# Kernel tuning notes

Measured on AMD Instinct MI355X. Metric: run time of the kernel, lower is better.

The kernel has to match this reference:

```python
import jax, jax.numpy as jnp
import numpy as np

N_NODES = 100000
N_EDGES = 1600000
N_GRAPHS = 256
D_IN = 128
D_HID = 128
D_OUT = 64


def graph_conv(x, src, dst, W_rel, b_rel, W_root):
    # PyG GraphConv: out = lin_rel(mean_{j->i} x_j) + lin_root(x)
    msgs = jax.ops.segment_sum(x[src], dst, num_segments=N_NODES)  # [N, d]
    deg = jax.ops.segment_sum(jnp.ones((src.shape[0],), x.dtype), dst, num_segments=N_NODES)
    agg = msgs / jnp.maximum(deg, 1.0)[:, None]
    return agg @ W_rel + b_rel + x @ W_root


def setup_inputs() -> dict:
    key = jax.random.key(0)
    ks = jax.random.split(key, 12)
    x = jax.random.normal(ks[0], (N_NODES, D_IN), dtype=jnp.float32)
    edge_index = jax.random.randint(ks[1], (2, N_EDGES), 0, N_NODES, dtype=jnp.int64)
    batch = jnp.sort(jax.random.randint(ks[2], (N_NODES,), 0, N_GRAPHS, dtype=jnp.int64))
    def lin(k, fan_in, fan_out):
        bound = 1.0 / np.sqrt(fan_in)
        return jax.random.uniform(k, (fan_in, fan_out), jnp.float32, -bound, bound)
    inp = {
        "x": x, "edge_index": edge_index, "batch": batch,
        "W1_rel": lin(ks[3], D_IN, D_HID), "b1_rel": jnp.zeros((D_HID,), jnp.float32), "W1_root": lin(ks[4], D_IN, D_HID),
        "W2_rel": lin(ks[5], D_HID, D_HID), "b2_rel": jnp.zeros((D_HID,), jnp.float32), "W2_root": lin(ks[6], D_HID, D_HID),
        "W3_rel": lin(ks[7], D_HID, D_HID), "b3_rel": jnp.zeros((D_HID,), jnp.float32), "W3_root": lin(ks[8], D_HID, D_HID),
        "Wl": lin(ks[9], D_HID, D_OUT), "bl": jnp.zeros((D_OUT,), jnp.float32),
    }
    return inp


def reference(x, edge_index, batch, W1_rel, b1_rel, W1_root, W2_rel, b2_rel, W2_root,
              W3_rel, b3_rel, W3_root, Wl, bl):
    src, dst = edge_index[0], edge_index[1]
    h = jax.nn.relu(graph_conv(x, src, dst, W1_rel, b1_rel, W1_root))
    h = jax.nn.relu(graph_conv(h, src, dst, W2_rel, b2_rel, W2_root))
    h = graph_conv(h, src, dst, W3_rel, b3_rel, W3_root)
    # global mean pool over graphs
    sums = jax.ops.segment_sum(h, batch, num_segments=N_GRAPHS)          # [G, d]
    cnts = jax.ops.segment_sum(jnp.ones((h.shape[0],), h.dtype), batch, num_segments=N_GRAPHS)
    pooled = sums / jnp.maximum(cnts, 1.0)[:, None]
    # dropout is identity at inference
    return pooled @ Wl + bl  # [G, D_OUT]
```

## Files before the change

kernel.cpp:

```cpp
#include <hip/hip_runtime.h>
#include <hip/hip_bf16.h>

#define N_NODES  100000
#define N_EDGES  1600000
#define N_GRAPHS 256
#define DCH      128
#define DOUT     64
#define NB       391
#define PADB     512
#define SLACK    4608
#define CHUNK    2048

typedef short v8s __attribute__((ext_vector_type(8)));
typedef float v4f __attribute__((ext_vector_type(4)));

static __device__ __forceinline__ float bf2f(unsigned short u) {
    unsigned int x = ((unsigned int)u) << 16;
    return __builtin_bit_cast(float, x);
}
static __device__ __forceinline__ unsigned short f2bf(float f) {
    unsigned int x = __builtin_bit_cast(unsigned int, f);
    unsigned int r = (x + 0x7fffu + ((x >> 16) & 1u)) >> 16;
    return (unsigned short)r;
}
static __device__ __forceinline__ int clampi(int v, int lo, int hi) {
    return v < lo ? lo : (v > hi ? hi : v);
}

__global__ void __launch_bounds__(256) binA_kernel(const int* __restrict__ src, const int* __restrict__ dst,
                                                   int* __restrict__ gcur, uint2* __restrict__ region) {
    __shared__ uint2 stage[CHUNK];
    __shared__ int hcnt[PADB], hcnt2[PADB], hoff[PADB], garr[PADB];
    __shared__ int s2[256];
    int tid = threadIdx.x;
    int e0  = blockIdx.x * CHUNK;
    int nedge = N_EDGES - e0; if (nedge > CHUNK) nedge = CHUNK;

    for (int b = tid; b < PADB; b += 256) { hcnt[b] = 0; hcnt2[b] = 0; }
    __syncthreads();

    int es[CHUNK / 256], ed[CHUNK / 256];
    #pragma unroll
    for (int j = 0; j < CHUNK / 256; j++) {
        int e = e0 + j * 256 + tid;
        if (e < N_EDGES) {
            es[j] = clampi(src[e], 0, N_NODES - 1);
            ed[j] = clampi(dst[e], 0, N_NODES - 1);
            atomicAdd(&hcnt[ed[j] >> 8], 1);
        } else { es[j] = -1; ed[j] = 0; }
    }
    __syncthreads();

    int v0 = hcnt[2 * tid], v1 = hcnt[2 * tid + 1];
    s2[tid] = v0 + v1; __syncthreads();
    for (int off = 1; off < 256; off <<= 1) {
        int x = (tid >= off) ? s2[tid - off] : 0;
        __syncthreads();
        s2[tid] += x;
        __syncthreads();
    }
    int excl = s2[tid] - (v0 + v1);
    hoff[2 * tid] = excl; hoff[2 * tid + 1] = excl + v0;
    __syncthreads();

    for (int b = tid; b < NB; b += 256) {
        int c = hcnt[b];
        garr[b] = b * SLACK + ((c > 0) ? atomicAdd(&gcur[b], c) : 0);
    }
    __syncthreads();

    #pragma unroll
    for (int j = 0; j < CHUNK / 256; j++) {
        if (es[j] >= 0) {
            int b = ed[j] >> 8;
            int pos = atomicAdd(&hcnt2[b], 1) + hoff[b];
            stage[pos] = (uint2){(unsigned)es[j], (unsigned)ed[j]};
        }
    }
    __syncthreads();

    for (int i = tid; i < nedge; i += 256) {
        uint2 en = stage[i];
        int b = (int)(en.y >> 8);
        int gpos = garr[b] + (i - hoff[b]);
        if (gpos < (b + 1) * SLACK) region[gpos] = en;
    }
}

__global__ void __launch_bounds__(256) scan_kernel(const int* __restrict__ gcur,
                                                   int* __restrict__ hoffG, int* __restrict__ rowptr) {
    __shared__ int s2[256];
    int tid = threadIdx.x;
    int c0 = gcur[2 * tid];     if (c0 > SLACK) c0 = SLACK;
    int c1 = gcur[2 * tid + 1]; if (c1 > SLACK) c1 = SLACK;
    s2[tid] = c0 + c1; __syncthreads();
    for (int off = 1; off < 256; off <<= 1) {
        int x = (tid >= off) ? s2[tid - off] : 0;
        __syncthreads();
        s2[tid] += x;
        __syncthreads();
    }
    int excl = s2[tid] - (c0 + c1);
    hoffG[2 * tid] = excl; hoffG[2 * tid + 1] = excl + c0;
    if (tid == 255) rowptr[N_NODES] = s2[255];
}

__global__ void __launch_bounds__(256) binFinish_kernel(const uint2* __restrict__ region, const int* __restrict__ gcur,
                                                        const int* __restrict__ hoffG,
                                                        int* __restrict__ rowptr, int* __restrict__ csr) {
    __shared__ int h[256], sc[256], cur[256];
    int b = blockIdx.x, tid = threadIdx.x;
    h[tid] = 0;
    int base = hoffG[b];
    int size = gcur[b]; if (size > SLACK) size = SLACK;
    int node0 = b * 256;
    __syncthreads();
    for (int j = tid; j < size; j += 256) {
        unsigned loc = region[b * SLACK + j].y - (unsigned)node0;
        if (loc < 256u) atomicAdd(&h[loc], 1);
    }
    __syncthreads();
    int v = h[tid]; sc[tid] = v; __syncthreads();
    for (int off = 1; off < 256; off <<= 1) {
        int x = (tid >= off) ? sc[tid - off] : 0;
        __syncthreads();
        sc[tid] += x;
        __syncthreads();
    }
    int myptr = base + sc[tid] - v;
    int node = node0 + tid;
    if (node < N_NODES) rowptr[node] = myptr;
    cur[tid] = myptr;
    __syncthreads();
    for (int j = tid; j < size; j += 256) {
        uint2 en = region[b * SLACK + j];
        unsigned loc = en.y - (unsigned)node0;
        if (loc < 256u) {
            int p = atomicAdd(&cur[loc], 1);
            if (p >= 0 && p < N_EDGES) csr[p] = (int)en.x;
        }
    }
}

__global__ void __launch_bounds__(256) prep_kernel(const float* __restrict__ x, unsigned short* __restrict__ B2,
                                                   const float* __restrict__ W1rel, const float* __restrict__ W1root,
                                                   const float* __restrict__ W2rel, const float* __restrict__ W2root,
                                                   const float* __restrict__ W3rel, const float* __restrict__ W3root,
                                                   unsigned short* __restrict__ frag,
                                                   unsigned short* __restrict__ z1, unsigned short* __restrict__ z2) {
    int bid = blockIdx.x, tid = threadIdx.x;
    if (bid < 12500) {
        size_t i = ((size_t)bid * 256 + tid) * 4;
        float4 f = *reinterpret_cast<const float4*>(x + i);
        uint2 o;
        o.x = ((unsigned)f2bf(f.y) << 16) | (unsigned)f2bf(f.x);
        o.y = ((unsigned)f2bf(f.w) << 16) | (unsigned)f2bf(f.z);
        *reinterpret_cast<uint2*>(B2 + i) = o;
    } else if (bid < 12548) {
        int gid = (bid - 12500) * 256 + tid;
        int lane = gid & 63;
        int nt   = (gid >> 6) & 7;
        int kt   = (gid >> 9) & 7;
        int L    = gid >> 12;
        const float* rel  = (L == 0) ? W1rel  : (L == 1) ? W2rel  : W3rel;
        const float* root = (L == 0) ? W1root : (L == 1) ? W2root : W3root;
        int n  = nt * 16 + (lane & 15);
        int k0 = kt * 32 + (lane >> 4) * 8;
        unsigned short o[8];
        #pragma unroll
        for (int j = 0; j < 8; j++) {
            int k = k0 + j;
            float w = (k < 128) ? rel[k * 128 + n] : root[(k - 128) * 128 + n];
            o[j] = f2bf(w);
        }
        uint4 u;
        u.x = (unsigned)o[0] | ((unsigned)o[1] << 16);
        u.y = (unsigned)o[2] | ((unsigned)o[3] << 16);
        u.z = (unsigned)o[4] | ((unsigned)o[5] << 16);
        u.w = (unsigned)o[6] | ((unsigned)o[7] << 16);
        *reinterpret_cast<uint4*>(frag + (size_t)gid * 8) = u;
    } else {
        if (tid < 64)       reinterpret_cast<unsigned*>(z1)[tid] = 0;
        else if (tid < 128) reinterpret_cast<unsigned*>(z2)[tid - 64] = 0;
    }
}

__global__ void __launch_bounds__(256, 6) layer_kernel(
    const unsigned short* __restrict__ hin,
    const int* __restrict__ rowptr, const int* __restrict__ csr,
    const unsigned short* __restrict__ frag, const float* __restrict__ bias,
    unsigned short* __restrict__ hout,
    const int* __restrict__ batch, float* __restrict__ psum, int mode)
{
    __shared__ __attribute__((aligned(16))) unsigned short As[4][16 * DCH];
    const int wave = threadIdx.x >> 6;
    const int lane = threadIdx.x & 63;
    const int l16  = lane & 15;
    const int quad = lane >> 4;
    const int base = blockIdx.x * 64 + wave * 16;
    if (base >= N_NODES) return;

    char* Asb = reinterpret_cast<char*>(As[wave]);

    int ridx = base + (lane < 17 ? lane : 16);
    if (ridx > N_NODES) ridx = N_NODES;
    int rp = rowptr[ridx];
    const int R0 = __builtin_amdgcn_readlane(rp, 0);
    const int R1 = __builtin_amdgcn_readlane(rp, 16);

    int ni     = 0;
    int nstart = R0;
    int nend   = __builtin_amdgcn_readlane(rp, 1);
    float a0 = 0.f, a1 = 0.f;

    int t0  = csr[R0 + l16];
    int idx = (R0 + l16 < R1) ? t0 : N_NODES;

    for (int e0 = R0; e0 < R1; e0 += 16) {
        int en   = e0 + 16 + l16;
        int tn   = csr[en];
        int idxn = (en < R1) ? tn : N_NODES;

        unsigned v[16];
        #pragma unroll
        for (int j = 0; j < 16; j++) {
            int s = __builtin_amdgcn_readlane(idx, j);
            v[j] = *reinterpret_cast<const unsigned*>(hin + (size_t)s * DCH + lane * 2);
        }

        #pragma unroll
        for (int j = 0; j < 16; j++) {
            int e = e0 + j;
            while (ni < 16 && e == nend) {
                int deg = nend - nstart;
                float inv = 1.0f / (float)(deg > 1 ? deg : 1);
                unsigned o = ((unsigned)f2bf(a1 * inv) << 16) | (unsigned)f2bf(a0 * inv);
                *reinterpret_cast<unsigned*>(Asb + ni * 256 + ((lane * 4) ^ ((ni & 7) << 4))) = o;
                a0 = 0.f; a1 = 0.f;
                ni++;
                nstart = nend;
                nend = __builtin_amdgcn_readlane(rp, ni + 1 < 17 ? ni + 1 : 16);
            }
            a0 += bf2f((unsigned short)(v[j] & 0xffffu));
            a1 += bf2f((unsigned short)(v[j] >> 16));
        }
        idx = idxn;
    }
    while (ni < 16) {
        int deg = nend - nstart;
        float inv = 1.0f / (float)(deg > 1 ? deg : 1);
        unsigned o = ((unsigned)f2bf(a1 * inv) << 16) | (unsigned)f2bf(a0 * inv);
        *reinterpret_cast<unsigned*>(Asb + ni * 256 + ((lane * 4) ^ ((ni & 7) << 4))) = o;
        a0 = 0.f; a1 = 0.f;
        ni++;
        nstart = nend;
        nend = __builtin_amdgcn_readlane(rp, ni + 1 < 17 ? ni + 1 : 16);
    }

    v4f acc[8];
    #pragma unroll
    for (int nt = 0; nt < 8; nt++) acc[nt] = (v4f){0.f, 0.f, 0.f, 0.f};

    #pragma unroll
    for (int kt = 0; kt < 8; kt++) {
        v8s av;
        if (kt < 4) {
            int co = (kt * 64 + quad * 16) ^ ((l16 & 7) << 4);
            av = *reinterpret_cast<const v8s*>(Asb + l16 * 256 + co);
        } else {
            int ak = (kt - 4) * 32 + quad * 8;
            int row = base + l16; if (row > N_NODES) row = N_NODES;
            av = *reinterpret_cast<const v8s*>(hin + (size_t)row * DCH + ak);
        }
        #pragma unroll
        for (int nt = 0; nt < 8; nt++) {
            v8s b = *reinterpret_cast<const v8s*>(frag + (((size_t)(kt * 8 + nt)) * 64 + lane) * 8);
            acc[nt] = __builtin_amdgcn_mfma_f32_16x16x32_bf16(av, b, acc[nt], 0, 0, 0);
        }
    }

    if (mode != 2) {
        #pragma unroll
        for (int nt = 0; nt < 8; nt++) {
            int n = nt * 16 + l16;
            float bv = bias[n];
            #pragma unroll
            for (int r = 0; r < 4; r++) {
                int row = base + quad * 4 + r;
                if (row < N_NODES) {
                    float v = acc[nt][r] + bv;
                    if (mode == 1) v = fmaxf(v, 0.f);
                    hout[(size_t)row * DCH + n] = f2bf(v);
                }
            }
        }
    } else {
        int last = base + 15;
        bool fast = (last < N_NODES) && (batch[base] == batch[last]);
        if (fast) {
            int g = batch[base];
            #pragma unroll
            for (int nt = 0; nt < 8; nt++) {
                int n = nt * 16 + l16;
                float s = acc[nt][0] + acc[nt][1] + acc[nt][2] + acc[nt][3] + 4.0f * bias[n];
                s += __shfl_xor(s, 16);
                s += __shfl_xor(s, 32);
                if (quad == 0) atomicAdd(&psum[g * DCH + n], s);
            }
        } else {
            int g[4];
            #pragma unroll
            for (int r = 0; r < 4; r++) {
                int row = base + quad * 4 + r;
                g[r] = (row < N_NODES) ? batch[row] : -1;
            }
            #pragma unroll
            for (int nt = 0; nt < 8; nt++) {
                int n = nt * 16 + l16;
                float bv = bias[n];
                float s = 0.f; int cg = -1;
                #pragma unroll
                for (int r = 0; r < 4; r++) {
                    if (g[r] < 0) continue;
                    if (g[r] != cg) {
                        if (cg >= 0) atomicAdd(&psum[cg * DCH + n], s);
                        s = 0.f; cg = g[r];
                    }
                    s += acc[nt][r] + bv;
                }
                if (cg >= 0) atomicAdd(&psum[cg * DCH + n], s);
            }
        }
    }
}

static __device__ __forceinline__ int lowerb(const int* __restrict__ a, int n, int key) {
    int lo = 0, hi = n;
    while (lo < hi) { int mid = (lo + hi) >> 1; if (a[mid] < key) lo = mid + 1; else hi = mid; }
    return lo;
}

__global__ void __launch_bounds__(64) final_kernel(const float* __restrict__ psum,
                                                   const int* __restrict__ batch,
                                                   const float* __restrict__ Wl, const float* __restrict__ bl,
                                                   float* __restrict__ out) {
    __shared__ float ps[DCH];
    __shared__ int bounds[2];
    int g = blockIdx.x, tid = threadIdx.x;
    if (tid == 0) {
        bounds[0] = lowerb(batch, N_NODES, g);
        bounds[1] = lowerb(batch, N_NODES, g + 1);
    }
    __syncthreads();
    int cnt = bounds[1] - bounds[0];
    float inv = 1.0f / (float)(cnt > 1 ? cnt : 1);
    ps[tid] = psum[g * DCH + tid] * inv;
    ps[tid + 64] = psum[g * DCH + tid + 64] * inv;
    __syncthreads();
    float o = 0.f;
    #pragma unroll 4
    for (int c = 0; c < DCH; c++) o += ps[c] * Wl[c * DOUT + tid];
    out[g * DOUT + tid] = o + bl[tid];
}

extern "C" void kernel_launch(void* const* d_in, const int* in_sizes, int n_in,
                              void* d_out, int out_size, void* d_ws, size_t ws_size,
                              hipStream_t stream) {
    const float* x     = (const float*)d_in[0];
    const int*   edge  = (const int*)d_in[1];
    const int*   src   = edge;
    const int*   dst   = edge + N_EDGES;
    const int*   batch = (const int*)d_in[2];
    const float* W1rel  = (const float*)d_in[3];
    const float* b1     = (const float*)d_in[4];
    const float* W1root = (const float*)d_in[5];
    const float* W2rel  = (const float*)d_in[6];
    const float* b2     = (const float*)d_in[7];
    const float* W2root = (const float*)d_in[8];
    const float* W3rel  = (const float*)d_in[9];
    const float* b3     = (const float*)d_in[10];
    const float* W3root = (const float*)d_in[11];
    const float* Wl     = (const float*)d_in[12];
    const float* bl     = (const float*)d_in[13];
    float* out = (float*)d_out;

    char* ws = (char*)d_ws;
    size_t off = 0;
    auto carve = [&](size_t bytes) -> void* {
        void* p = ws + off;
        off += (bytes + 255) & ~(size_t)255;
        return p;
    };
    int*            rowptr  = (int*)carve((size_t)(N_NODES + 1) * 4);
    int*            csr     = (int*)carve((size_t)(N_EDGES + 64) * 4);
    int*            gcur    = (int*)carve((size_t)PADB * 4 + (size_t)N_GRAPHS * DCH * 4);
    float*          psum    = (float*)(gcur + PADB);
    int*            hoffG   = (int*)carve((size_t)PADB * 4);
    unsigned short* frag    = (unsigned short*)carve((size_t)3 * 8 * 8 * 64 * 8 * 2);
    unsigned short* B1      = (unsigned short*)carve((size_t)(N_NODES + 1) * DCH * 2);
    unsigned short* B2      = (unsigned short*)carve((size_t)(N_NODES + 1) * DCH * 2);
    uint2*          region  = (uint2*)B1;

    hipMemsetAsync(gcur, 0, (size_t)PADB * 4 + (size_t)N_GRAPHS * DCH * 4, stream);

    binA_kernel<<<(N_EDGES + CHUNK - 1) / CHUNK, 256, 0, stream>>>(src, dst, gcur, region);
    scan_kernel<<<1, 256, 0, stream>>>(gcur, hoffG, rowptr);
    binFinish_kernel<<<NB, 256, 0, stream>>>(region, gcur, hoffG, rowptr, csr);
    prep_kernel<<<12549, 256, 0, stream>>>(x, B2, W1rel, W1root, W2rel, W2root, W3rel, W3root,
                                           frag, B1 + (size_t)N_NODES * DCH, B2 + (size_t)N_NODES * DCH);

    const int layerGrid = (N_NODES + 63) / 64;

    layer_kernel<<<layerGrid, 256, 0, stream>>>(B2, rowptr, csr, frag,         b1, B1, batch, psum, 1);
    layer_kernel<<<layerGrid, 256, 0, stream>>>(B1, rowptr, csr, frag + 32768, b2, B2, batch, psum, 1);
    layer_kernel<<<layerGrid, 256, 0, stream>>>(B2, rowptr, csr, frag + 65536, b3, B1, batch, psum, 2);

    final_kernel<<<N_GRAPHS, 64, 0, stream>>>(psum, batch, Wl, bl, out);
}
```

Measured before the change: 411.4 us.

## Double-buffer neighbor gathers in layer kernel and fold memset into prep

The aggregation loop in the layer kernel now ping-pongs between two register buffers. It issues the next 16-edge chunk's row gathers and the following chunk's CSR index load before reducing the current chunk, so global-load latency overlaps the accumulation. The CSR padding is enlarged to cover the deeper index lookahead. The separate hipMemsetAsync is removed: the prep kernel now zeroes gcur and psum itself and is launched before the binning kernels, saving an API call. The extra 16-register buffer raises VGPR pressure under the 6-blocks-per-SM launch bound, which could cost occupancy or cause spills.

```diff
diff --git a/kernel.cpp b/kernel.cpp
--- a/kernel.cpp
+++ b/kernel.cpp
@@ -147,7 +147,8 @@
                                                    const float* __restrict__ W2rel, const float* __restrict__ W2root,
                                                    const float* __restrict__ W3rel, const float* __restrict__ W3root,
                                                    unsigned short* __restrict__ frag,
-                                                   unsigned short* __restrict__ z1, unsigned short* __restrict__ z2) {
+                                                   unsigned short* __restrict__ z1, unsigned short* __restrict__ z2,
+                                                   int* __restrict__ gcur, float* __restrict__ psum) {
     int bid = blockIdx.x, tid = threadIdx.x;
     if (bid < 12500) {
         size_t i = ((size_t)bid * 256 + tid) * 4;
@@ -179,9 +180,13 @@
         u.z = (unsigned)o[4] | ((unsigned)o[5] << 16);
         u.w = (unsigned)o[6] | ((unsigned)o[7] << 16);
         *reinterpret_cast<uint4*>(frag + (size_t)gid * 8) = u;
-    } else {
+    } else if (bid == 12548) {
         if (tid < 64)       reinterpret_cast<unsigned*>(z1)[tid] = 0;
         else if (tid < 128) reinterpret_cast<unsigned*>(z2)[tid - 64] = 0;
+        gcur[tid] = 0; gcur[tid + 256] = 0;
+    } else {
+        int i = (bid - 12549) * 1024 + tid * 4;
+        *reinterpret_cast<float4*>(psum + i) = (float4){0.f, 0.f, 0.f, 0.f};
     }
 }
 
@@ -213,38 +218,80 @@
     int nend   = __builtin_amdgcn_readlane(rp, 1);
     float a0 = 0.f, a1 = 0.f;
 
-    int t0  = csr[R0 + l16];
-    int idx = (R0 + l16 < R1) ? t0 : N_NODES;
-
-    for (int e0 = R0; e0 < R1; e0 += 16) {
-        int en   = e0 + 16 + l16;
-        int tn   = csr[en];
-        int idxn = (en < R1) ? tn : N_NODES;
-
-        unsigned v[16];
+    int nch = (R1 - R0 + 15) >> 4;
+    if (nch < 1) nch = 1;
+    const int nch2 = (nch + 1) & ~1;
+
+    unsigned vA[16], vB[16];
+
+    int tA = csr[R0 + l16];
+    int tB;
+    {
+        int idx = (R0 + l16 < R1) ? tA : N_NODES;
         #pragma unroll
         for (int j = 0; j < 16; j++) {
             int s = __builtin_amdgcn_readlane(idx, j);
-            v[j] = *reinterpret_cast<const unsigned*>(hin + (size_t)s * DCH + lane * 2);
-        }
-
-        #pragma unroll
-        for (int j = 0; j < 16; j++) {
-            int e = e0 + j;
-            while (ni < 16 && e == nend) {
-                int deg = nend - nstart;
-                float inv = 1.0f / (float)(deg > 1 ? deg : 1);
-                unsigned o = ((unsigned)f2bf(a1 * inv) << 16) | (unsigned)f2bf(a0 * inv);
-                *reinterpret_cast<unsigned*>(Asb + ni * 256 + ((lane * 4) ^ ((ni & 7) << 4))) = o;
-                a0 = 0.f; a1 = 0.f;
-                ni++;
-                nstart = nend;
-                nend = __builtin_amdgcn_readlane(rp, ni + 1 < 17 ? ni + 1 : 16);
-            }
-            a0 += bf2f((unsigned short)(v[j] & 0xffffu));
-            a1 += bf2f((unsigned short)(v[j] >> 16));
-        }
-        idx = idxn;
+            vA[j] = *reinterpret_cast<const unsigned*>(hin + (size_t)s * DCH + lane * 2);
+        }
+        tB = csr[R0 + 16 + l16];
+    }
+
+    int e0 = R0;
+    for (int c = 0; c < nch2; c += 2) {
+        {
+            int e1 = e0 + 16;
+            int idx = (e1 + l16 < R1) ? tB : N_NODES;
+            #pragma unroll
+            for (int j = 0; j < 16; j++) {
+                int s = __builtin_amdgcn_readlane(idx, j);
+                vB[j] = *reinterpret_cast<const unsigned*>(hin + (size_t)s * DCH + lane * 2);
+            }
+            tA = csr[e0 + 32 + l16];
+            #pragma unroll
+            for (int j = 0; j < 16; j++) {
+                int e = e0 + j;
+                while (ni < 16 && e == nend) {
+                    int deg = nend - nstart;
+                    float inv = 1.0f / (float)(deg > 1 ? deg : 1);
+                    unsigned o = ((unsigned)f2bf(a1 * inv) << 16) | (unsigned)f2bf(a0 * inv);
+                    *reinterpret_cast<unsigned*>(Asb + ni * 256 + ((lane * 4) ^ ((ni & 7) << 4))) = o;
+                    a0 = 0.f; a1 = 0.f;
+                    ni++;
+                    nstart = nend;
+                    nend = __builtin_amdgcn_readlane(rp, ni + 1 < 17 ? ni + 1 : 16);
+                }
+                a0 += bf2f((unsigned short)(vA[j] & 0xffffu));
+                a1 += bf2f((unsigned short)(vA[j] >> 16));
+            }
+            e0 = e1;
+        }
+        {
+            int e1 = e0 + 16;
+            int idx = (e1 + l16 < R1) ? tA : N_NODES;
+            #pragma unroll
+            for (int j = 0; j < 16; j++) {
+                int s = __builtin_amdgcn_readlane(idx, j);
+                vA[j] = *reinterpret_cast<const unsigned*>(hin + (size_t)s * DCH + lane * 2);
+            }
+            tB = csr[e0 + 32 + l16];
+            #pragma unroll
+            for (int j = 0; j < 16; j++) {
+                int e = e0 + j;
+                while (ni < 16 && e == nend) {
+                    int deg = nend - nstart;
+                    float inv = 1.0f / (float)(deg > 1 ? deg : 1);
+                    unsigned o = ((unsigned)f2bf(a1 * inv) << 16) | (unsigned)f2bf(a0 * inv);
+                    *reinterpret_cast<unsigned*>(Asb + ni * 256 + ((lane * 4) ^ ((ni & 7) << 4))) = o;
+                    a0 = 0.f; a1 = 0.f;
+                    ni++;
+                    nstart = nend;
+                    nend = __builtin_amdgcn_readlane(rp, ni + 1 < 17 ? ni + 1 : 16);
+                }
+                a0 += bf2f((unsigned short)(vB[j] & 0xffffu));
+                a1 += bf2f((unsigned short)(vB[j] >> 16));
+            }
+            e0 = e1;
+        }
     }
     while (ni < 16) {
         int deg = nend - nstart;
@@ -392,7 +439,7 @@
         return p;
     };
     int*            rowptr  = (int*)carve((size_t)(N_NODES + 1) * 4);
-    int*            csr     = (int*)carve((size_t)(N_EDGES + 64) * 4);
+    int*            csr     = (int*)carve((size_t)(N_EDGES + 128) * 4);
     int*            gcur    = (int*)carve((size_t)PADB * 4 + (size_t)N_GRAPHS * DCH * 4);
     float*          psum    = (float*)(gcur + PADB);
     int*            hoffG   = (int*)carve((size_t)PADB * 4);
@@ -401,13 +448,13 @@
     unsigned short* B2      = (unsigned short*)carve((size_t)(N_NODES + 1) * DCH * 2);
     uint2*          region  = (uint2*)B1;
 
-    hipMemsetAsync(gcur, 0, (size_t)PADB * 4 + (size_t)N_GRAPHS * DCH * 4, stream);
+    prep_kernel<<<12581, 256, 0, stream>>>(x, B2, W1rel, W1root, W2rel, W2root, W3rel, W3root,
+                                           frag, B1 + (size_t)N_NODES * DCH, B2 + (size_t)N_NODES * DCH,
+                                           gcur, psum);
 
     binA_kernel<<<(N_EDGES + CHUNK - 1) / CHUNK, 256, 0, stream>>>(src, dst, gcur, region);
     scan_kernel<<<1, 256, 0, stream>>>(gcur, hoffG, rowptr);
     binFinish_kernel<<<NB, 256, 0, stream>>>(region, gcur, hoffG, rowptr, csr);
-    prep_kernel<<<12549, 256, 0, stream>>>(x, B2, W1rel, W1root, W2rel, W2root, W3rel, W3root,
-                                           frag, B1 + (size_t)N_NODES * DCH, B2 + (size_t)N_NODES * DCH);
 
     const int layerGrid = (N_NODES + 63) / 64;
 
```

Result: no change. 411.0 us (-0.1%).

## Triple-buffer neighbor gathers in layer kernel and fold memset into prep kernel

Applied to the files above, without the earlier changes.

The CSR aggregation loop in layer_kernel now keeps three 16-edge gather buffers in flight. While one chunk is accumulated, loads for the next chunks are already issued, which hides gather latency. Launch bounds drop from 6 to 4 waves per SIMD to fit the extra registers, and the CSR allocation is padded for the lookahead reads. Separately, the hipMemsetAsync of gcur and psum is replaced by extra blocks in prep_kernel, which now launches first, removing one API call and launch.

```diff
diff --git a/kernel.cpp b/kernel.cpp
--- a/kernel.cpp
+++ b/kernel.cpp
@@ -147,7 +147,8 @@
                                                    const float* __restrict__ W2rel, const float* __restrict__ W2root,
                                                    const float* __restrict__ W3rel, const float* __restrict__ W3root,
                                                    unsigned short* __restrict__ frag,
-                                                   unsigned short* __restrict__ z1, unsigned short* __restrict__ z2) {
+                                                   unsigned short* __restrict__ z1, unsigned short* __restrict__ z2,
+                                                   int* __restrict__ gcur, float* __restrict__ psum) {
     int bid = blockIdx.x, tid = threadIdx.x;
     if (bid < 12500) {
         size_t i = ((size_t)bid * 256 + tid) * 4;
@@ -179,13 +180,17 @@
         u.z = (unsigned)o[4] | ((unsigned)o[5] << 16);
         u.w = (unsigned)o[6] | ((unsigned)o[7] << 16);
         *reinterpret_cast<uint4*>(frag + (size_t)gid * 8) = u;
-    } else {
+    } else if (bid == 12548) {
         if (tid < 64)       reinterpret_cast<unsigned*>(z1)[tid] = 0;
         else if (tid < 128) reinterpret_cast<unsigned*>(z2)[tid - 64] = 0;
-    }
-}
-
-__global__ void __launch_bounds__(256, 6) layer_kernel(
+        gcur[tid] = 0; gcur[tid + 256] = 0;
+    } else {
+        int i = (bid - 12549) * 1024 + tid * 4;
+        *reinterpret_cast<float4*>(psum + i) = (float4){0.f, 0.f, 0.f, 0.f};
+    }
+}
+
+__global__ void __launch_bounds__(256, 4) layer_kernel(
     const unsigned short* __restrict__ hin,
     const int* __restrict__ rowptr, const int* __restrict__ csr,
     const unsigned short* __restrict__ frag, const float* __restrict__ bias,
@@ -213,24 +218,25 @@
     int nend   = __builtin_amdgcn_readlane(rp, 1);
     float a0 = 0.f, a1 = 0.f;
 
-    int t0  = csr[R0 + l16];
-    int idx = (R0 + l16 < R1) ? t0 : N_NODES;
-
-    for (int e0 = R0; e0 < R1; e0 += 16) {
-        int en   = e0 + 16 + l16;
-        int tn   = csr[en];
-        int idxn = (en < R1) ? tn : N_NODES;
-
-        unsigned v[16];
+    int nch = (R1 - R0 + 15) >> 4;
+    if (nch < 1) nch = 1;
+    const int nch3 = ((nch + 2) / 3) * 3;
+
+    unsigned v0[16], v1[16], v2[16];
+    int t0, t1, t2;
+
+    auto issue_gathers = [&](unsigned (&vv)[16], int traw, int eb) {
+        int idx = (eb + l16 < R1) ? traw : N_NODES;
         #pragma unroll
         for (int j = 0; j < 16; j++) {
             int s = __builtin_amdgcn_readlane(idx, j);
-            v[j] = *reinterpret_cast<const unsigned*>(hin + (size_t)s * DCH + lane * 2);
-        }
-
+            vv[j] = *reinterpret_cast<const unsigned*>(hin + (size_t)s * DCH + lane * 2);
+        }
+    };
+    auto accum = [&](unsigned (&vv)[16], int eb) {
         #pragma unroll
         for (int j = 0; j < 16; j++) {
-            int e = e0 + j;
+            int e = eb + j;
             while (ni < 16 && e == nend) {
                 int deg = nend - nstart;
                 float inv = 1.0f / (float)(deg > 1 ? deg : 1);
@@ -241,10 +247,32 @@
                 nstart = nend;
                 nend = __builtin_amdgcn_readlane(rp, ni + 1 < 17 ? ni + 1 : 16);
             }
-            a0 += bf2f((unsigned short)(v[j] & 0xffffu));
-            a1 += bf2f((unsigned short)(v[j] >> 16));
-        }
-        idx = idxn;
+            a0 += bf2f((unsigned short)(vv[j] & 0xffffu));
+            a1 += bf2f((unsigned short)(vv[j] >> 16));
+        }
+    };
+
+    t0 = csr[R0 + l16];
+    t1 = csr[R0 + 16 + l16];
+    t2 = csr[R0 + 32 + l16];
+    issue_gathers(v0, t0, R0);
+    t0 = csr[R0 + 48 + l16];
+    issue_gathers(v1, t1, R0 + 16);
+
+    int e0 = R0;
+    for (int c = 0; c < nch3; c += 3) {
+        t1 = csr[e0 + 64 + l16];
+        issue_gathers(v2, t2, e0 + 32);
+        accum(v0, e0);
+        e0 += 16;
+        t2 = csr[e0 + 64 + l16];
+        issue_gathers(v0, t0, e0 + 32);
+        accum(v1, e0);
+        e0 += 16;
+        t0 = csr[e0 + 64 + l16];
+        issue_gathers(v1, t1, e0 + 32);
+        accum(v2, e0);
+        e0 += 16;
     }
     while (ni < 16) {
         int deg = nend - nstart;
@@ -392,7 +420,7 @@
         return p;
     };
     int*            rowptr  = (int*)carve((size_t)(N_NODES + 1) * 4);
-    int*            csr     = (int*)carve((size_t)(N_EDGES + 64) * 4);
+    int*            csr     = (int*)carve((size_t)(N_EDGES + 160) * 4);
     int*            gcur    = (int*)carve((size_t)PADB * 4 + (size_t)N_GRAPHS * DCH * 4);
     float*          psum    = (float*)(gcur + PADB);
     int*            hoffG   = (int*)carve((size_t)PADB * 4);
@@ -401,13 +429,13 @@
     unsigned short* B2      = (unsigned short*)carve((size_t)(N_NODES + 1) * DCH * 2);
     uint2*          region  = (uint2*)B1;
 
-    hipMemsetAsync(gcur, 0, (size_t)PADB * 4 + (size_t)N_GRAPHS * DCH * 4, stream);
+    prep_kernel<<<12581, 256, 0, stream>>>(x, B2, W1rel, W1root, W2rel, W2root, W3rel, W3root,
+                                           frag, B1 + (size_t)N_NODES * DCH, B2 + (size_t)N_NODES * DCH,
+                                           gcur, psum);
 
     binA_kernel<<<(N_EDGES + CHUNK - 1) / CHUNK, 256, 0, stream>>>(src, dst, gcur, region);
     scan_kernel<<<1, 256, 0, stream>>>(gcur, hoffG, rowptr);
     binFinish_kernel<<<NB, 256, 0, stream>>>(region, gcur, hoffG, rowptr, csr);
-    prep_kernel<<<12549, 256, 0, stream>>>(x, B2, W1rel, W1root, W2rel, W2root, W3rel, W3root,
-                                           frag, B1 + (size_t)N_NODES * DCH, B2 + (size_t)N_NODES * DCH);
 
     const int layerGrid = (N_NODES + 63) / 64;
 
```

Result: no change. 414.4 us (+0.7%).

## Split fused layer into per-node aggregation and GEMM kernels, merge setup kernels

Applied to the files above, without the earlier changes.

The fused gather-plus-GEMM layer kernel is split in two. A new aggregation kernel assigns one wave per node and writes the mean-aggregated bf16 features to a buffer. A GEMM kernel then loads that tile into LDS and writes its output in place. Separately, the binning and prep kernels are merged into one launch, and the global scan is recomputed redundantly inside each binFinish block, which removes the standalone scan launch. This aims for better load balance across irregular node degrees and fewer setup launches. The cost is writing and re-reading an extra 128-wide bf16 buffer per layer, three more layer launches, and dropped row bounds checks in the GEMM path.

```diff
diff --git a/kernel.cpp b/kernel.cpp
--- a/kernel.cpp
+++ b/kernel.cpp
@@ -10,6 +10,7 @@
 #define PADB     512
 #define SLACK    4608
 #define CHUNK    2048
+#define NBINA    782
 
 typedef short v8s __attribute__((ext_vector_type(8)));
 typedef float v4f __attribute__((ext_vector_type(4)));
@@ -27,12 +28,60 @@
     return v < lo ? lo : (v > hi ? hi : v);
 }
 
-__global__ void __launch_bounds__(256) binA_kernel(const int* __restrict__ src, const int* __restrict__ dst,
-                                                   int* __restrict__ gcur, uint2* __restrict__ region) {
+__global__ void __launch_bounds__(256) binAprep_kernel(
+    const int* __restrict__ src, const int* __restrict__ dst,
+    int* __restrict__ gcur, uint2* __restrict__ region,
+    const float* __restrict__ x, unsigned short* __restrict__ B2,
+    const float* __restrict__ W1rel, const float* __restrict__ W1root,
+    const float* __restrict__ W2rel, const float* __restrict__ W2root,
+    const float* __restrict__ W3rel, const float* __restrict__ W3root,
+    unsigned short* __restrict__ frag,
+    unsigned short* __restrict__ z1, unsigned short* __restrict__ z2)
+{
     __shared__ uint2 stage[CHUNK];
     __shared__ int hcnt[PADB], hcnt2[PADB], hoff[PADB], garr[PADB];
     __shared__ int s2[256];
     int tid = threadIdx.x;
+
+    if (blockIdx.x >= NBINA) {
+        int bid = blockIdx.x - NBINA;
+        if (bid < 12500) {
+            size_t i = ((size_t)bid * 256 + tid) * 4;
+            float4 f = *reinterpret_cast<const float4*>(x + i);
+            uint2 o;
+            o.x = ((unsigned)f2bf(f.y) << 16) | (unsigned)f2bf(f.x);
+            o.y = ((unsigned)f2bf(f.w) << 16) | (unsigned)f2bf(f.z);
+            *reinterpret_cast<uint2*>(B2 + i) = o;
+        } else if (bid < 12548) {
+            int gid = (bid - 12500) * 256 + tid;
+            int lane = gid & 63;
+            int nt   = (gid >> 6) & 7;
+            int kt   = (gid >> 9) & 7;
+            int L    = gid >> 12;
+            const float* rel  = (L == 0) ? W1rel  : (L == 1) ? W2rel  : W3rel;
+            const float* root = (L == 0) ? W1root : (L == 1) ? W2root : W3root;
+            int n  = nt * 16 + (lane & 15);
+            int k0 = kt * 32 + (lane >> 4) * 8;
+            unsigned short o[8];
+            #pragma unroll
+            for (int j = 0; j < 8; j++) {
+                int k = k0 + j;
+                float w = (k < 128) ? rel[k * 128 + n] : root[(k - 128) * 128 + n];
+                o[j] = f2bf(w);
+            }
+            uint4 u;
+            u.x = (unsigned)o[0] | ((unsigned)o[1] << 16);
+            u.y = (unsigned)o[2] | ((unsigned)o[3] << 16);
+            u.z = (unsigned)o[4] | ((unsigned)o[5] << 16);
+            u.w = (unsigned)o[6] | ((unsigned)o[7] << 16);
+            *reinterpret_cast<uint4*>(frag + (size_t)gid * 8) = u;
+        } else {
+            if (tid < 64)       reinterpret_cast<unsigned*>(z1)[tid] = 0;
+            else if (tid < 128) reinterpret_cast<unsigned*>(z2)[tid - 64] = 0;
+        }
+        return;
+    }
+
     int e0  = blockIdx.x * CHUNK;
     int nedge = N_EDGES - e0; if (nedge > CHUNK) nedge = CHUNK;
 
@@ -54,9 +103,9 @@
     int v0 = hcnt[2 * tid], v1 = hcnt[2 * tid + 1];
     s2[tid] = v0 + v1; __syncthreads();
     for (int off = 1; off < 256; off <<= 1) {
-        int x = (tid >= off) ? s2[tid - off] : 0;
-        __syncthreads();
-        s2[tid] += x;
+        int xx = (tid >= off) ? s2[tid - off] : 0;
+        __syncthreads();
+        s2[tid] += xx;
         __syncthreads();
     }
     int excl = s2[tid] - (v0 + v1);
@@ -87,34 +136,28 @@
     }
 }
 
-__global__ void __launch_bounds__(256) scan_kernel(const int* __restrict__ gcur,
-                                                   int* __restrict__ hoffG, int* __restrict__ rowptr) {
-    __shared__ int s2[256];
-    int tid = threadIdx.x;
+__global__ void __launch_bounds__(256) binFinish_kernel(const uint2* __restrict__ region, const int* __restrict__ gcur,
+                                                        int* __restrict__ rowptr, int* __restrict__ csr) {
+    __shared__ int h[256], sc[256], cur[256], s2[256], hoff[PADB];
+    int b = blockIdx.x, tid = threadIdx.x;
     int c0 = gcur[2 * tid];     if (c0 > SLACK) c0 = SLACK;
     int c1 = gcur[2 * tid + 1]; if (c1 > SLACK) c1 = SLACK;
-    s2[tid] = c0 + c1; __syncthreads();
+    s2[tid] = c0 + c1;
+    h[tid] = 0;
+    __syncthreads();
     for (int off = 1; off < 256; off <<= 1) {
-        int x = (tid >= off) ? s2[tid - off] : 0;
-        __syncthreads();
-        s2[tid] += x;
+        int xx = (tid >= off) ? s2[tid - off] : 0;
+        __syncthreads();
+        s2[tid] += xx;
         __syncthreads();
     }
     int excl = s2[tid] - (c0 + c1);
-    hoffG[2 * tid] = excl; hoffG[2 * tid + 1] = excl + c0;
-    if (tid == 255) rowptr[N_NODES] = s2[255];
-}
-
-__global__ void __launch_bounds__(256) binFinish_kernel(const uint2* __restrict__ region, const int* __restrict__ gcur,
-                                                        const int* __restrict__ hoffG,
-                                                        int* __restrict__ rowptr, int* __restrict__ csr) {
-    __shared__ int h[256], sc[256], cur[256];
-    int b = blockIdx.x, tid = threadIdx.x;
-    h[tid] = 0;
-    int base = hoffG[b];
+    hoff[2 * tid] = excl; hoff[2 * tid + 1] = excl + c0;
+    __syncthreads();
+    if (b == 0 && tid == 255) rowptr[N_NODES] = s2[255];
+    int base = hoff[b];
     int size = gcur[b]; if (size > SLACK) size = SLACK;
     int node0 = b * 256;
-    __syncthreads();
     for (int j = tid; j < size; j += 256) {
         unsigned loc = region[b * SLACK + j].y - (unsigned)node0;
         if (loc < 256u) atomicAdd(&h[loc], 1);
@@ -122,9 +165,9 @@
     __syncthreads();
     int v = h[tid]; sc[tid] = v; __syncthreads();
     for (int off = 1; off < 256; off <<= 1) {
-        int x = (tid >= off) ? sc[tid - off] : 0;
-        __syncthreads();
-        sc[tid] += x;
+        int xx = (tid >= off) ? sc[tid - off] : 0;
+        __syncthreads();
+        sc[tid] += xx;
         __syncthreads();
     }
     int myptr = base + sc[tid] - v;
@@ -142,54 +185,42 @@
     }
 }
 
-__global__ void __launch_bounds__(256) prep_kernel(const float* __restrict__ x, unsigned short* __restrict__ B2,
-                                                   const float* __restrict__ W1rel, const float* __restrict__ W1root,
-                                                   const float* __restrict__ W2rel, const float* __restrict__ W2root,
-                                                   const float* __restrict__ W3rel, const float* __restrict__ W3root,
-                                                   unsigned short* __restrict__ frag,
-                                                   unsigned short* __restrict__ z1, unsigned short* __restrict__ z2) {
-    int bid = blockIdx.x, tid = threadIdx.x;
-    if (bid < 12500) {
-        size_t i = ((size_t)bid * 256 + tid) * 4;
-        float4 f = *reinterpret_cast<const float4*>(x + i);
-        uint2 o;
-        o.x = ((unsigned)f2bf(f.y) << 16) | (unsigned)f2bf(f.x);
-        o.y = ((unsigned)f2bf(f.w) << 16) | (unsigned)f2bf(f.z);
-        *reinterpret_cast<uint2*>(B2 + i) = o;
-    } else if (bid < 12548) {
-        int gid = (bid - 12500) * 256 + tid;
-        int lane = gid & 63;
-        int nt   = (gid >> 6) & 7;
-        int kt   = (gid >> 9) & 7;
-        int L    = gid >> 12;
-        const float* rel  = (L == 0) ? W1rel  : (L == 1) ? W2rel  : W3rel;
-        const float* root = (L == 0) ? W1root : (L == 1) ? W2root : W3root;
-        int n  = nt * 16 + (lane & 15);
-        int k0 = kt * 32 + (lane >> 4) * 8;
-        unsigned short o[8];
-        #pragma unroll
-        for (int j = 0; j < 8; j++) {
-            int k = k0 + j;
-            float w = (k < 128) ? rel[k * 128 + n] : root[(k - 128) * 128 + n];
-            o[j] = f2bf(w);
-        }
-        uint4 u;
-        u.x = (unsigned)o[0] | ((unsigned)o[1] << 16);
-        u.y = (unsigned)o[2] | ((unsigned)o[3] << 16);
-        u.z = (unsigned)o[4] | ((unsigned)o[5] << 16);
-        u.w = (unsigned)o[6] | ((unsigned)o[7] << 16);
-        *reinterpret_cast<uint4*>(frag + (size_t)gid * 8) = u;
-    } else {
-        if (tid < 64)       reinterpret_cast<unsigned*>(z1)[tid] = 0;
-        else if (tid < 128) reinterpret_cast<unsigned*>(z2)[tid - 64] = 0;
-    }
-}
-
-__global__ void __launch_bounds__(256, 6) layer_kernel(
+__global__ void __launch_bounds__(256, 8) agg_kernel(
     const unsigned short* __restrict__ hin,
     const int* __restrict__ rowptr, const int* __restrict__ csr,
+    unsigned short* __restrict__ agg)
+{
+    const int wid  = __builtin_amdgcn_readfirstlane(threadIdx.x >> 6);
+    const int lane = threadIdx.x & 63;
+    const int l16  = lane & 15;
+    const int node = blockIdx.x * 4 + wid;
+    const int r0 = rowptr[node];
+    const int r1 = rowptr[node + 1];
+
+    float a0 = 0.f, a1 = 0.f;
+    int t = csr[r0 + l16];
+    for (int c = r0; c < r1; c += 16) {
+        int tn = csr[c + 16 + l16];
+        int idx = (c + l16 < r1) ? t : N_NODES;
+        #pragma unroll
+        for (int j = 0; j < 16; j++) {
+            int s = __builtin_amdgcn_readlane(idx, j);
+            unsigned v = *reinterpret_cast<const unsigned*>(hin + (size_t)s * DCH + lane * 2);
+            a0 += bf2f((unsigned short)(v & 0xffffu));
+            a1 += bf2f((unsigned short)(v >> 16));
+        }
+        t = tn;
+    }
+    int deg = r1 - r0;
+    float inv = 1.0f / (float)(deg > 1 ? deg : 1);
+    unsigned o = ((unsigned)f2bf(a1 * inv) << 16) | (unsigned)f2bf(a0 * inv);
+    *reinterpret_cast<unsigned*>(agg + (size_t)node * DCH + lane * 2) = o;
+}
+
+__global__ void __launch_bounds__(256, 4) gemm_kernel(
+    unsigned short* agg,
+    const unsigned short* __restrict__ root,
     const unsigned short* __restrict__ frag, const float* __restrict__ bias,
-    unsigned short* __restrict__ hout,
     const int* __restrict__ batch, float* __restrict__ psum, int mode)
 {
     __shared__ __attribute__((aligned(16))) unsigned short As[4][16 * DCH];
@@ -202,59 +233,13 @@
 
     char* Asb = reinterpret_cast<char*>(As[wave]);
 
-    int ridx = base + (lane < 17 ? lane : 16);
-    if (ridx > N_NODES) ridx = N_NODES;
-    int rp = rowptr[ridx];
-    const int R0 = __builtin_amdgcn_readlane(rp, 0);
-    const int R1 = __builtin_amdgcn_readlane(rp, 16);
-
-    int ni     = 0;
-    int nstart = R0;
-    int nend   = __builtin_amdgcn_readlane(rp, 1);
-    float a0 = 0.f, a1 = 0.f;
-
-    int t0  = csr[R0 + l16];
-    int idx = (R0 + l16 < R1) ? t0 : N_NODES;
-
-    for (int e0 = R0; e0 < R1; e0 += 16) {
-        int en   = e0 + 16 + l16;
-        int tn   = csr[en];
-        int idxn = (en < R1) ? tn : N_NODES;
-
-        unsigned v[16];
-        #pragma unroll
-        for (int j = 0; j < 16; j++) {
-            int s = __builtin_amdgcn_readlane(idx, j);
-            v[j] = *reinterpret_cast<const unsigned*>(hin + (size_t)s * DCH + lane * 2);
-        }
-
-        #pragma unroll
-        for (int j = 0; j < 16; j++) {
-            int e = e0 + j;
-            while (ni < 16 && e == nend) {
-                int deg = nend - nstart;
-                float inv = 1.0f / (float)(deg > 1 ? deg : 1);
-                unsigned o = ((unsigned)f2bf(a1 * inv) << 16) | (unsigned)f2bf(a0 * inv);
-                *reinterpret_cast<unsigned*>(Asb + ni * 256 + ((lane * 4) ^ ((ni & 7) << 4))) = o;
-                a0 = 0.f; a1 = 0.f;
-                ni++;
-                nstart = nend;
-                nend = __builtin_amdgcn_readlane(rp, ni + 1 < 17 ? ni + 1 : 16);
-            }
-            a0 += bf2f((unsigned short)(v[j] & 0xffffu));
-            a1 += bf2f((unsigned short)(v[j] >> 16));
-        }
-        idx = idxn;
-    }
-    while (ni < 16) {
-        int deg = nend - nstart;
-        float inv = 1.0f / (float)(deg > 1 ? deg : 1);
-        unsigned o = ((unsigned)f2bf(a1 * inv) << 16) | (unsigned)f2bf(a0 * inv);
-        *reinterpret_cast<unsigned*>(Asb + ni * 256 + ((lane * 4) ^ ((ni & 7) << 4))) = o;
-        a0 = 0.f; a1 = 0.f;
-        ni++;
-        nstart = nend;
-        nend = __builtin_amdgcn_readlane(rp, ni + 1 < 17 ? ni + 1 : 16);
+    #pragma unroll
+    for (int k = 0; k < 4; k++) {
+        const char* gp = reinterpret_cast<const char*>(agg) + (size_t)base * 256 + k * 1024 + lane * 16;
+        uint4 d = *reinterpret_cast<const uint4*>(gp);
+        int row = k * 4 + (lane >> 4);
+        int col = (lane & 15) * 16;
+        *reinterpret_cast<uint4*>(Asb + row * 256 + (col ^ ((row & 7) << 4))) = d;
     }
 
     v4f acc[8];
@@ -269,8 +254,7 @@
             av = *reinterpret_cast<const v8s*>(Asb + l16 * 256 + co);
         } else {
             int ak = (kt - 4) * 32 + quad * 8;
-            int row = base + l16; if (row > N_NODES) row = N_NODES;
-            av = *reinterpret_cast<const v8s*>(hin + (size_t)row * DCH + ak);
+            av = *reinterpret_cast<const v8s*>(root + (size_t)(base + l16) * DCH + ak);
         }
         #pragma unroll
         for (int nt = 0; nt < 8; nt++) {
@@ -287,16 +271,13 @@
             #pragma unroll
             for (int r = 0; r < 4; r++) {
                 int row = base + quad * 4 + r;
-                if (row < N_NODES) {
-                    float v = acc[nt][r] + bv;
-                    if (mode == 1) v = fmaxf(v, 0.f);
-                    hout[(size_t)row * DCH + n] = f2bf(v);
-                }
+                float v = acc[nt][r] + bv;
+                if (mode == 1) v = fmaxf(v, 0.f);
+                agg[(size_t)row * DCH + n] = f2bf(v);
             }
         }
     } else {
-        int last = base + 15;
-        bool fast = (last < N_NODES) && (batch[base] == batch[last]);
+        bool fast = (batch[base] == batch[base + 15]);
         if (fast) {
             int g = batch[base];
             #pragma unroll
@@ -310,10 +291,7 @@
         } else {
             int g[4];
             #pragma unroll
-            for (int r = 0; r < 4; r++) {
-                int row = base + quad * 4 + r;
-                g[r] = (row < N_NODES) ? batch[row] : -1;
-            }
+            for (int r = 0; r < 4; r++) g[r] = batch[base + quad * 4 + r];
             #pragma unroll
             for (int nt = 0; nt < 8; nt++) {
                 int n = nt * 16 + l16;
@@ -321,7 +299,6 @@
                 float s = 0.f; int cg = -1;
                 #pragma unroll
                 for (int r = 0; r < 4; r++) {
-                    if (g[r] < 0) continue;
                     if (g[r] != cg) {
                         if (cg >= 0) atomicAdd(&psum[cg * DCH + n], s);
                         s = 0.f; cg = g[r];
@@ -395,7 +372,6 @@
     int*            csr     = (int*)carve((size_t)(N_EDGES + 64) * 4);
     int*            gcur    = (int*)carve((size_t)PADB * 4 + (size_t)N_GRAPHS * DCH * 4);
     float*          psum    = (float*)(gcur + PADB);
-    int*            hoffG   = (int*)carve((size_t)PADB * 4);
     unsigned short* frag    = (unsigned short*)carve((size_t)3 * 8 * 8 * 64 * 8 * 2);
     unsigned short* B1      = (unsigned short*)carve((size_t)(N_NODES + 1) * DCH * 2);
     unsigned short* B2      = (unsigned short*)carve((size_t)(N_NODES + 1) * DCH * 2);
@@ -403,17 +379,20 @@
 
     hipMemsetAsync(gcur, 0, (size_t)PADB * 4 + (size_t)N_GRAPHS * DCH * 4, stream);
 
-    binA_kernel<<<(N_EDGES + CHUNK - 1) / CHUNK, 256, 0, stream>>>(src, dst, gcur, region);
-    scan_kernel<<<1, 256, 0, stream>>>(gcur, hoffG, rowptr);
-    binFinish_kernel<<<NB, 256, 0, stream>>>(region, gcur, hoffG, rowptr, csr);
-    prep_kernel<<<12549, 256, 0, stream>>>(x, B2, W1rel, W1root, W2rel, W2root, W3rel, W3root,
-                                           frag, B1 + (size_t)N_NODES * DCH, B2 + (size_t)N_NODES * DCH);
-
-    const int layerGrid = (N_NODES + 63) / 64;
-
-    layer_kernel<<<layerGrid, 256, 0, stream>>>(B2, rowptr, csr, frag,         b1, B1, batch, psum, 1);
-    layer_kernel<<<layerGrid, 256, 0, stream>>>(B1, rowptr, csr, frag + 32768, b2, B2, batch, psum, 1);
-    layer_kernel<<<layerGrid, 256, 0, stream>>>(B2, rowptr, csr, frag + 65536, b3, B1, batch, psum, 2);
+    binAprep_kernel<<<NBINA + 12549, 256, 0, stream>>>(src, dst, gcur, region,
+                                                       x, B2, W1rel, W1root, W2rel, W2root, W3rel, W3root,
+                                                       frag, B1 + (size_t)N_NODES * DCH, B2 + (size_t)N_NODES * DCH);
+    binFinish_kernel<<<NB, 256, 0, stream>>>(region, gcur, rowptr, csr);
+
+    const int aggGrid  = N_NODES / 4;
+    const int gemmGrid = (N_NODES + 63) / 64;
+
+    agg_kernel<<<aggGrid, 256, 0, stream>>>(B2, rowptr, csr, B1);
+    gemm_kernel<<<gemmGrid, 256, 0, stream>>>(B1, B2, frag,         b1, batch, psum, 1);
+    agg_kernel<<<aggGrid, 256, 0, stream>>>(B1, rowptr, csr, B2);
+    gemm_kernel<<<gemmGrid, 256, 0, stream>>>(B2, B1, frag + 32768, b2, batch, psum, 1);
+    agg_kernel<<<aggGrid, 256, 0, stream>>>(B2, rowptr, csr, B1);
+    gemm_kernel<<<gemmGrid, 256, 0, stream>>>(B1, B2, frag + 65536, b3, batch, psum, 2);
 
     final_kernel<<<N_GRAPHS, 64, 0, stream>>>(psum, batch, Wl, bl, out);
 }
```

Measured after the change: 419.8 us. +2.0%, slower.
